# Kernel tuning notes

Measured on AMD Instinct MI355X. Metric: run time of the kernel, lower is better.

Reference implementation:

```python
import jax, jax.numpy as jnp
from jax import lax
import numpy as np

B = 32768
N_IN = 8
N_HID = 64
N_CTRL = 2
M_SCEN = (1.0, 1.2)          # scenario parameters for f/g
M_NOM = 1.0
CLF_LAM = 1.0
CBF_LAM = 1.0
P_CLF = 100.0
P_CBF = 50.0
QP_ITERS = 80                # fixed-iteration batched ADMM (OSQP-style) replacing CvxpyLayer
RHO = 1.0
SIGMA = 1e-6
INF = jnp.inf


def setup_inputs() -> dict:
    key = jax.random.key(0)
    ks = jax.random.split(key, 16)
    s = 0.3
    return {
        "x":   jax.random.normal(ks[0], (B, N_IN), jnp.float32),
        "VW1": jax.random.normal(ks[1], (N_HID, N_IN), jnp.float32) * s,
        "Vb1": jax.random.normal(ks[2], (N_HID,), jnp.float32) * s,
        "VW2": jax.random.normal(ks[3], (N_HID, N_HID), jnp.float32) * s,
        "Vb2": jax.random.normal(ks[4], (N_HID,), jnp.float32) * s,
        "HW1": jax.random.normal(ks[5], (N_HID, N_IN), jnp.float32) * s,
        "Hb1": jax.random.normal(ks[6], (N_HID,), jnp.float32) * s,
        "HW2": jax.random.normal(ks[7], (N_HID, N_HID), jnp.float32) * s,
        "Hb2": jax.random.normal(ks[8], (N_HID,), jnp.float32) * s,
        "HW3": jax.random.normal(ks[9], (N_HID, N_HID), jnp.float32) * s,
        "Hb3": jax.random.normal(ks[10], (N_HID,), jnp.float32) * s,
        "HW4": jax.random.normal(ks[11], (1, N_HID), jnp.float32) * s,
        "Hb4": jax.random.normal(ks[12], (1,), jnp.float32) * s,
        "G0":  jax.random.normal(ks[13], (N_IN, N_CTRL), jnp.float32) * s,
        "K":   jax.random.normal(ks[14], (N_IN, N_CTRL), jnp.float32) * s,
    }


def _lyapunov(x, W1, b1, W2, b2):
    t1 = jnp.tanh(x @ W1.T + b1)                                   # [B,H]
    t2 = jnp.tanh(t1 @ W2.T + b2)                                  # [B,H]
    V = 0.5 * jnp.sum(t2 * t2, axis=1)                             # [B]
    # fused diag(1-t^2) @ W chain (no diag_embed materialization)
    D1 = (1.0 - t1 ** 2)[:, :, None] * W1[None]                    # [B,H,N]
    D2 = (1.0 - t2 ** 2)[:, :, None] * jnp.einsum('hk,bkn->bhn', W2, D1)
    grad_V = jnp.einsum('bh,bhn->bn', t2, D2)                      # [B,N]
    return V, grad_V


def _barrier(x, W1, b1, W2, b2, W3, b3, W4, b4):
    t1 = jnp.tanh(x @ W1.T + b1)
    t2 = jnp.tanh(t1 @ W2.T + b2)
    t3 = jnp.tanh(t2 @ W3.T + b3)
    H = t3 @ W4.T + b4                                             # [B,1]
    D1 = (1.0 - t1 ** 2)[:, :, None] * W1[None]
    D2 = (1.0 - t2 ** 2)[:, :, None] * jnp.einsum('hk,bkn->bhn', W2, D1)
    D3 = (1.0 - t3 ** 2)[:, :, None] * jnp.einsum('hk,bkn->bhn', W3, D2)
    grad_H = jnp.einsum('oh,bhn->bn', W4, D3)                      # [B,N] (o=1)
    return H, grad_H


def _solve_qp(q, A, lo, hi):
    """Batched OSQP-style ADMM for min 0.5 z^T P z + q^T z  s.t. lo <= A z <= hi.
    P = diag([2,2,0,0,0,0]); z = [u(2), r_clf(2), s_cbf(2)]. Fixed iterations."""
    nb, mc, nz = A.shape[0], A.shape[1], A.shape[2]
    Pdiag = jnp.array([2.0, 2.0, 0.0, 0.0, 0.0, 0.0], q.dtype)
    M = RHO * jnp.einsum('bmi,bmj->bij', A, A) + jnp.diag(Pdiag + SIGMA)
    Minv = jnp.linalg.inv(M)                                       # [B,6,6]
    x0 = jnp.zeros((nb, nz), q.dtype)
    z0 = jnp.zeros((nb, mc), q.dtype)
    y0 = jnp.zeros((nb, mc), q.dtype)

    def step(carry, _):
        xx, zz, yy = carry
        rhs = SIGMA * xx - q + jnp.einsum('bmi,bm->bi', A, RHO * zz - yy)
        xt = jnp.einsum('bij,bj->bi', Minv, rhs)
        zt = jnp.einsum('bmi,bi->bm', A, xt)
        zn = jnp.clip(zt + yy / RHO, lo, hi)
        yn = yy + RHO * (zt - zn)
        return (xt, zn, yn), None

    (xf, _, _), _ = lax.scan(step, (x0, z0, y0), None, length=QP_ITERS)
    return xf                                                      # [B,6]


def _forward(x, VW1, Vb1, VW2, Vb2, HW1, Hb1, HW2, Hb2, HW3, Hb3, HW4, Hb4, G0, K):
    V, grad_V = _lyapunov(x, VW1, Vb1, VW2, Vb2)
    H, grad_H = _barrier(x, HW1, Hb1, HW2, Hb2, HW3, Hb3, HW4, Hb4)

    LfVs, LgVs, LfHs, LgHs = [], [], [], []
    for m in M_SCEN:
        # f(x,m) = -x/m ; g(x,m) = G0/m
        LfVs.append(-jnp.sum(grad_V * x, axis=1) / m)              # [B]
        LgVs.append((grad_V @ G0) / m)                             # [B,C]
        LfHs.append(-jnp.sum(grad_H * x, axis=1) / m)
        LgHs.append((grad_H @ G0) / m)
    u_nom = -(x @ K) * (1.0 / M_NOM)                               # [B,C]

    nb = x.shape[0]
    z2 = jnp.zeros((nb, 2), x.dtype)
    ey = jnp.eye(2, dtype=x.dtype)
    e = lambda i: jnp.broadcast_to(ey[i], (nb, 2))
    ninf = jnp.full((nb,), -INF, x.dtype)
    pinf = jnp.full((nb,), INF, x.dtype)
    zer = jnp.zeros((nb,), x.dtype)

    rows, los, his = [], [], []
    for i in range(len(M_SCEN)):
        # CBF: LfH + LgH@u + cbf_lam*H + s_i >= 0
        rows.append(jnp.concatenate([LgHs[i], z2, e(i)], axis=1))
        los.append(-(LfHs[i] + CBF_LAM * H[:, 0])); his.append(pinf)
        # CLF: LfV + LgV@u + clf_lam*V - r_i <= 0
        rows.append(jnp.concatenate([LgVs[i], -e(i), z2], axis=1))
        los.append(ninf); his.append(-(LfVs[i] + CLF_LAM * V))
    for i in range(len(M_SCEN)):
        rows.append(jnp.concatenate([z2, e(i), z2], axis=1)); los.append(zer); his.append(pinf)
    for i in range(len(M_SCEN)):
        rows.append(jnp.concatenate([z2, z2, e(i)], axis=1)); los.append(zer); his.append(pinf)

    A = jnp.stack(rows, axis=1)                                    # [B,8,6]
    lo = jnp.stack(los, axis=1)                                    # [B,8]
    hi = jnp.stack(his, axis=1)
    # objective ||u-u_nom||^2 + p_clf*sum r + p_cbf*sum s  ->  q = [-2 u_nom, p_clf, p_clf, p_cbf, p_cbf]
    q = jnp.concatenate([-2.0 * u_nom,
                         jnp.full((nb, 2), P_CLF, x.dtype),
                         jnp.full((nb, 2), P_CBF, x.dtype)], axis=1)

    z = _solve_qp(q, A, lo, hi)                                    # [B,6]
    u = z[:, :N_CTRL]
    relaxation = jnp.mean(z[:, N_CTRL:N_CTRL + len(M_SCEN)], axis=1, keepdims=True)  # [B,1]

    ns = float(len(M_SCEN))
    Vdot = sum(LfVs[i] + jnp.sum(LgVs[i] * u, axis=1) for i in range(len(M_SCEN))) / ns
    Hdot = sum(LfHs[i] + jnp.sum(LgHs[i] * u, axis=1) for i in range(len(M_SCEN))) / ns
    return u, relaxation, V, Vdot[:, None, None], H, Hdot[:, None, None]


def reference(x, VW1, Vb1, VW2, Vb2, HW1, Hb1, HW2, Hb2, HW3, Hb3, HW4, Hb4, G0, K):
    return _forward(x, VW1, Vb1, VW2, Vb2, HW1, Hb1, HW2, Hb2, HW3, Hb3, HW4, Hb4, G0, K)
```

## Files before the change

### kernel.cpp

```cpp
#include <hip/hip_runtime.h>
#include <hip/hip_bf16.h>
#include <math.h>

#define BTOT 32768

typedef _Float16 f16x8 __attribute__((ext_vector_type(8)));
typedef _Float16 f16x4 __attribute__((ext_vector_type(4)));
typedef float    f32x4 __attribute__((ext_vector_type(4)));

#define LDS_FENCE() asm volatile("s_waitcnt lgkmcnt(0)" ::: "memory")

__device__ __forceinline__ float ldin(const void* p, int i, int f32f) {
  return f32f ? ((const float*)p)[i]
              : __bfloat162float(((const __hip_bfloat16*)p)[i]);
}

__device__ __forceinline__ f32x4 MFMA(f16x8 a, f16x8 b, f32x4 c) {
  return __builtin_amdgcn_mfma_f32_16x16x32_f16(a, b, c, 0, 0, 0);
}

__device__ __forceinline__ float tanh_fast(float x) {
  float e = __expf(2.f * x);
  return 1.f - 2.f * __builtin_amdgcn_rcpf(e + 1.f);
}

__device__ __forceinline__ float redq(float v) {
  v += __shfl_xor(v, 16, 64);
  v += __shfl_xor(v, 32, 64);
  return v;
}

__device__ __forceinline__ int widx(int h, int k) {
  return ((h >> 4) << 10) + ((k >> 5) << 9) + (((k >> 3) & 3) << 7) + ((h & 15) << 3) + (k & 7);
}

__global__ __launch_bounds__(512, 4) void fused_kernel(
    const void* px, const void* pVW1, const void* pVb1, const void* pVW2, const void* pVb2,
    const void* pHW1, const void* pHb1, const void* pHW2, const void* pHb2,
    const void* pHW3, const void* pHb3, const void* pHW4, const void* pHb4,
    const void* pG0, const void* pK, float* out)
{
  __shared__ __align__(16) _Float16 sVW2[4096], sVW2T[4096];
  __shared__ __align__(16) _Float16 sHW2[4096], sHW2T[4096];
  __shared__ __align__(16) _Float16 sHW3[4096], sHW3T[4096];
  __shared__ __align__(16) _Float16 sW1Vh[512], sW1Vl[512], sW1Hh[512], sW1Hl[512];
  __shared__ __align__(16) _Float16 sAct[8][1024];
  __shared__ __align__(16) float sVb1[64], sVb2[64], sHb1[64], sHb2[64], sHb3[64], sW4[64];
  __shared__ __align__(16) float sWGV0[64], sWGV1[64], sWGH0[64], sWGH1[64];
  __shared__ __align__(16) float sQP[128][11];
  __shared__ float sKv[16], sHb4v;
  __shared__ int sCnt;

  const int tid = threadIdx.x, lane = tid & 63, wave = tid >> 6;
  const int m = lane & 15, q = lane >> 4;
  const int ro = q * 128 + m * 8;

  if (tid == 0) sCnt = 0;
  __syncthreads();
  {
    const unsigned short* xb = (const unsigned short*)px;
    int good = 0;
#pragma unroll
    for (int i = 0; i < 2; ++i) {
      int ex = (xb[tid * 2 + i] >> 7) & 0xFF;
      good += (ex >= 97 && ex <= 157) ? 1 : 0;
    }
    atomicAdd(&sCnt, good);
  }
  __syncthreads();
  const int f32f = (sCnt >= 870) ? 0 : 1;
  const bool wsplit = (f32f != 0);

  for (int i = tid; i < 4096; i += 512) {
    int h = i >> 6, k = i & 63;
    int fw = widx(h, k), tw = widx(k, h);
    sVW2[fw] = (_Float16)ldin(pVW2, i, f32f); sVW2T[tw] = sVW2[fw];
    sHW2[fw] = (_Float16)ldin(pHW2, i, f32f); sHW2T[tw] = sHW2[fw];
    sHW3[fw] = (_Float16)ldin(pHW3, i, f32f); sHW3T[tw] = sHW3[fw];
  }
  for (int i = tid; i < 512; i += 512) {
    float v = ldin(pVW1, i, f32f); _Float16 hh = (_Float16)v;
    sW1Vh[i] = hh; sW1Vl[i] = (_Float16)(v - (float)hh);
    v = ldin(pHW1, i, f32f); hh = (_Float16)v;
    sW1Hh[i] = hh; sW1Hl[i] = (_Float16)(v - (float)hh);
  }
  if (tid < 64) {
    float a0 = 0.f, a1 = 0.f, b0 = 0.f, b1 = 0.f;
#pragma unroll
    for (int nn = 0; nn < 8; ++nn) {
      float g0 = ldin(pG0, 2 * nn, f32f), g1 = ldin(pG0, 2 * nn + 1, f32f);
      float wv = ldin(pVW1, tid * 8 + nn, f32f), wh = ldin(pHW1, tid * 8 + nn, f32f);
      a0 += wv * g0; a1 += wv * g1; b0 += wh * g0; b1 += wh * g1;
    }
    sWGV0[tid] = a0; sWGV1[tid] = a1; sWGH0[tid] = b0; sWGH1[tid] = b1;
    sVb1[tid] = ldin(pVb1, tid, f32f);
    sVb2[tid] = ldin(pVb2, tid, f32f);
    sHb1[tid] = ldin(pHb1, tid, f32f);
    sHb2[tid] = ldin(pHb2, tid, f32f);
    sHb3[tid] = ldin(pHb3, tid, f32f);
    sW4[tid]  = ldin(pHW4, tid, f32f);
  }
  if (tid < 16) sKv[tid] = ldin(pK, tid, f32f);
  if (tid == 0) sHb4v = ldin(pHb4, 0, f32f);
  __syncthreads();

  f16x8 zf;
#pragma unroll
  for (int i = 0; i < 8; ++i) zf[i] = (_Float16)0.f;

  _Float16* act = sAct[wave];
  const int tb = wave * 16;
  const int e0 = blockIdx.x * 128 + tb;

  f16x8 xbh = zf, xbl = zf;
  if (lane < 16) {
#pragma unroll
    for (int n = 0; n < 8; ++n) {
      float v = ldin(px, (e0 + m) * 8 + n, f32f);
      _Float16 hh = (_Float16)v;
      xbh[n] = hh; xbl[n] = (_Float16)(v - (float)hh);
    }
  }

  auto wgemm = [&](const _Float16* Wp, f32x4* acc) {
    f16x8 b0 = *(const f16x8*)(act + ro);
    f16x8 b1 = *(const f16x8*)(act + 512 + ro);
#pragma unroll
    for (int ht = 0; ht < 4; ++ht) {
      const _Float16* ap = Wp + ht * 1024 + ro;
      f32x4 c = {0.f, 0.f, 0.f, 0.f};
      c = MFMA(*(const f16x8*)ap, b0, c);
      c = MFMA(*(const f16x8*)(ap + 512), b1, c);
      acc[ht] = c;
    }
  };
  auto wstore = [&](const f32x4* vals) {
#pragma unroll
    for (int ht = 0; ht < 4; ++ht) {
      int aw = ((ht >> 1) << 9) + (((ht & 1) * 2 + (q >> 1)) << 7) + m * 8 + ((q & 1) << 2);
      f16x4 vh;
#pragma unroll
      for (int r = 0; r < 4; ++r) vh[r] = (_Float16)vals[ht][r];
      *(f16x4*)(act + aw) = vh;
    }
  };
  auto l1gemm = [&](const _Float16* W1h, const _Float16* W1l, f32x4* acc) {
#pragma unroll
    for (int ht = 0; ht < 4; ++ht) {
      f16x8 afh = zf, afl = zf;
      if (lane < 16) {
        afh = *(const f16x8*)(W1h + (ht * 16 + m) * 8);
        afl = *(const f16x8*)(W1l + (ht * 16 + m) * 8);
      }
      f32x4 c = {0.f, 0.f, 0.f, 0.f};
      c = MFMA(afh, xbh, c);
      c = MFMA(afh, xbl, c);
      if (wsplit) c = MFMA(afl, xbh, c);
      acc[ht] = c;
    }
  };

  f32x4 acc[4], z1[4], d1[4], d2[4], tv[4];

  l1gemm(sW1Vh, sW1Vl, acc);
#pragma unroll
  for (int ht = 0; ht < 4; ++ht) {
    z1[ht] = acc[ht];
    f32x4 b4 = *(const f32x4*)&sVb1[ht * 16 + q * 4];
#pragma unroll
    for (int r = 0; r < 4; ++r) {
      float t = tanh_fast(z1[ht][r] + b4[r]);
      tv[ht][r] = t; d1[ht][r] = 1.f - t * t;
    }
  }
  wstore(tv); LDS_FENCE();

  wgemm(sVW2, acc);
  float pV = 0.f;
#pragma unroll
  for (int ht = 0; ht < 4; ++ht) {
    f32x4 b4 = *(const f32x4*)&sVb2[ht * 16 + q * 4];
#pragma unroll
    for (int r = 0; r < 4; ++r) {
      float t = tanh_fast(acc[ht][r] + b4[r]);
      pV += t * t;
      tv[ht][r] = t * (1.f - t * t);
    }
  }
  wstore(tv); LDS_FENCE();

  wgemm(sVW2T, acc);
  float pgvx = 0.f, plv0 = 0.f, plv1 = 0.f;
#pragma unroll
  for (int ht = 0; ht < 4; ++ht) {
    f32x4 g0 = *(const f32x4*)&sWGV0[ht * 16 + q * 4];
    f32x4 g1 = *(const f32x4*)&sWGV1[ht * 16 + q * 4];
#pragma unroll
    for (int r = 0; r < 4; ++r) {
      float wt = acc[ht][r] * d1[ht][r];
      pgvx += wt * z1[ht][r];
      plv0 += wt * g0[r]; plv1 += wt * g1[r];
    }
  }

  l1gemm(sW1Hh, sW1Hl, acc);
#pragma unroll
  for (int ht = 0; ht < 4; ++ht) {
    z1[ht] = acc[ht];
    f32x4 b4 = *(const f32x4*)&sHb1[ht * 16 + q * 4];
#pragma unroll
    for (int r = 0; r < 4; ++r) {
      float t = tanh_fast(z1[ht][r] + b4[r]);
      tv[ht][r] = t; d1[ht][r] = 1.f - t * t;
    }
  }
  wstore(tv); LDS_FENCE();

  wgemm(sHW2, acc);
#pragma unroll
  for (int ht = 0; ht < 4; ++ht) {
    f32x4 b4 = *(const f32x4*)&sHb2[ht * 16 + q * 4];
#pragma unroll
    for (int r = 0; r < 4; ++r) {
      float t = tanh_fast(acc[ht][r] + b4[r]);
      tv[ht][r] = t; d2[ht][r] = 1.f - t * t;
    }
  }
  wstore(tv); LDS_FENCE();

  wgemm(sHW3, acc);
  float pH = 0.f;
#pragma unroll
  for (int ht = 0; ht < 4; ++ht) {
    f32x4 b4 = *(const f32x4*)&sHb3[ht * 16 + q * 4];
    f32x4 w4 = *(const f32x4*)&sW4[ht * 16 + q * 4];
#pragma unroll
    for (int r = 0; r < 4; ++r) {
      float t = tanh_fast(acc[ht][r] + b4[r]);
      pH += t * w4[r];
      tv[ht][r] = w4[r] * (1.f - t * t);
    }
  }
  wstore(tv); LDS_FENCE();

  wgemm(sHW3T, acc);
#pragma unroll
  for (int ht = 0; ht < 4; ++ht)
#pragma unroll
    for (int r = 0; r < 4; ++r) tv[ht][r] = acc[ht][r] * d2[ht][r];
  wstore(tv); LDS_FENCE();

  wgemm(sHW2T, acc);
  float pghx = 0.f, plh0 = 0.f, plh1 = 0.f;
#pragma unroll
  for (int ht = 0; ht < 4; ++ht) {
    f32x4 g0 = *(const f32x4*)&sWGH0[ht * 16 + q * 4];
    f32x4 g1 = *(const f32x4*)&sWGH1[ht * 16 + q * 4];
#pragma unroll
    for (int r = 0; r < 4; ++r) {
      float wt = acc[ht][r] * d1[ht][r];
      pghx += wt * z1[ht][r];
      plh0 += wt * g0[r]; plh1 += wt * g1[r];
    }
  }

  {
    float rgvx = redq(pgvx), rlv0 = redq(plv0), rlv1 = redq(plv1), rV = 0.5f * redq(pV);
    float rghx = redq(pghx), rlh0 = redq(plh0), rlh1 = redq(plh1), rH = redq(pH) + sHb4v;
    if (lane < 16) {
      int el = tb + lane;
      sQP[el][0] = rlh0;  sQP[el][1] = rlh1;
      sQP[el][2] = rlv0;  sQP[el][3] = rlv1;
      sQP[el][4] = rghx;  sQP[el][5] = rgvx;
      sQP[el][6] = rV;    sQP[el][7] = rH;
      out[98304 + e0 + lane]  = rV;
      out[163840 + e0 + lane] = rH;
    }
  }
  __syncthreads();

  if (tid >= 128) return;
  const int e = blockIdx.x * 128 + tid;
  const float im = 1.0f / 1.2f;
  const float sg = 1e-6f;

  float gh0 = sQP[tid][0], gh1 = sQP[tid][1];
  float gv0 = sQP[tid][2], gv1 = sQP[tid][3];
  float ghx = sQP[tid][4], gvx = sQP[tid][5];
  float V   = sQP[tid][6], H   = sQP[tid][7];

  float un0 = 0.f, un1 = 0.f;
#pragma unroll
  for (int n = 0; n < 8; ++n) {
    float xv = ldin(px, e * 8 + n, f32f);
    un0 -= xv * sKv[2 * n];
    un1 -= xv * sKv[2 * n + 1];
  }

  float lo0 = ghx - H;
  float hi1 = gvx - V;
  float lo2 = ghx * im - H;
  float hi3 = gvx * im - V;
  float qv0 = -2.f * un0, qv1 = -2.f * un1;

  const float d  = 2.f + sg;
  const float rd = 1.f / d;
  const float al = 1.f + im * im;
  const float be = al * (1.f - rd);
  float S00 = be * (gh0 * gh0 + gv0 * gv0) + d;
  float S11 = be * (gh1 * gh1 + gv1 * gv1) + d;
  float S01 = be * (gh0 * gh1 + gv0 * gv1);
  float idet = 1.f / (S00 * S11 - S01 * S01);
  float i00 = S11 * idet, i11 = S00 * idet, i01 = -S01 * idet;

  float X0 = 0.f, X1 = 0.f, X2 = 0.f, X3 = 0.f, X4 = 0.f, X5 = 0.f;
  float Z[8] = {0.f, 0.f, 0.f, 0.f, 0.f, 0.f, 0.f, 0.f};
  float Y[8] = {0.f, 0.f, 0.f, 0.f, 0.f, 0.f, 0.f, 0.f};

#pragma unroll 1
  for (int it = 0; it < 80; ++it) {
    float t0 = Z[0] - Y[0], t1 = Z[1] - Y[1], t2 = Z[2] - Y[2], t3 = Z[3] - Y[3];
    float t4 = Z[4] - Y[4], t5 = Z[5] - Y[5], t6 = Z[6] - Y[6], t7 = Z[7] - Y[7];
    float tauh = t0 + im * t2, tauv = t1 + im * t3;
    float b0 = sg * X0 - qv0 + gh0 * tauh + gv0 * tauv;
    float b1 = sg * X1 - qv1 + gh1 * tauh + gv1 * tauv;
    float b2 = sg * X2 - 100.f - t1 + t4;
    float b3 = sg * X3 - 100.f - t3 + t5;
    float b4 = sg * X4 - 50.f + t0 + t6;
    float b5 = sg * X5 - 50.f + t2 + t7;
    float p  = b2 + im * b3;
    float s2 = b4 + im * b5;
    float cb0 = gh0 * s2 - gv0 * p;
    float cb1 = gh1 * s2 - gv1 * p;
    float u0b = b0 - cb0 * rd;
    float u1b = b1 - cb1 * rd;
    X0 = i00 * u0b + i01 * u1b;
    X1 = i01 * u0b + i11 * u1b;
    float gdH = gh0 * X0 + gh1 * X1;
    float gdV = gv0 * X0 + gv1 * X1;
    X2 = (b2 + gdV) * rd;
    X3 = (b3 + im * gdV) * rd;
    X4 = (b4 - gdH) * rd;
    X5 = (b5 - im * gdH) * rd;
    float zt0 = gdH + X4;
    float zt1 = gdV - X2;
    float zt2 = gdH * im + X5;
    float zt3 = gdV * im - X3;

    float v, zn;
    v = zt0 + Y[0]; zn = fmaxf(v, lo0); Y[0] += zt0 - zn; Z[0] = zn;
    v = zt1 + Y[1]; zn = fminf(v, hi1); Y[1] += zt1 - zn; Z[1] = zn;
    v = zt2 + Y[2]; zn = fmaxf(v, lo2); Y[2] += zt2 - zn; Z[2] = zn;
    v = zt3 + Y[3]; zn = fminf(v, hi3); Y[3] += zt3 - zn; Z[3] = zn;
    v = X2 + Y[4];  zn = fmaxf(v, 0.f); Y[4] += X2 - zn;  Z[4] = zn;
    v = X3 + Y[5];  zn = fmaxf(v, 0.f); Y[5] += X3 - zn;  Z[5] = zn;
    v = X4 + Y[6];  zn = fmaxf(v, 0.f); Y[6] += X4 - zn;  Z[6] = zn;
    v = X5 + Y[7];  zn = fmaxf(v, 0.f); Y[7] += X5 - zn;  Z[7] = zn;
  }

  float relax = 0.5f * (X2 + X3);
  const float cc = 0.5f * (1.f + im);
  float Vdot = cc * (gv0 * X0 + gv1 * X1 - gvx);
  float Hdot = cc * (gh0 * X0 + gh1 * X1 - ghx);

  out[2 * e]      = X0;
  out[2 * e + 1]  = X1;
  out[65536 + e]  = relax;
  out[131072 + e] = Vdot;
  out[196608 + e] = Hdot;
}

extern "C" void kernel_launch(void* const* d_in, const int* in_sizes, int n_in,
                              void* d_out, int out_size, void* d_ws, size_t ws_size,
                              hipStream_t stream) {
  float* out = (float*)d_out;
  fused_kernel<<<256, 512, 0, stream>>>(
      d_in[0], d_in[1], d_in[2], d_in[3], d_in[4],
      d_in[5], d_in[6], d_in[7], d_in[8],
      d_in[9], d_in[10], d_in[11], d_in[12],
      d_in[13], d_in[14], out);
}
```

Measured before the change: 121.6 us.

## Split weight prep into separate kernel and process 16 rows per small block

Weight conversion and transposition to f16 MFMA layout moves into a prep kernel that writes to workspace, so each block no longer redoes it in shared memory. The main kernel now uses 2048 blocks of 128 threads, each handling 16 rows with the hidden dimension split across two waves. The V and H networks are interleaved so their independent GEMMs can overlap, and weights are read from global memory/cache instead of LDS. The cost is an extra launch, block-level barriers between layers, and a final QP stage that uses only 16 threads per block.

```diff
diff --git a/kernel.cpp b/kernel.cpp
--- a/kernel.cpp
+++ b/kernel.cpp
@@ -7,8 +7,6 @@
 typedef _Float16 f16x8 __attribute__((ext_vector_type(8)));
 typedef _Float16 f16x4 __attribute__((ext_vector_type(4)));
 typedef float    f32x4 __attribute__((ext_vector_type(4)));
-
-#define LDS_FENCE() asm volatile("s_waitcnt lgkmcnt(0)" ::: "memory")
 
 __device__ __forceinline__ float ldin(const void* p, int i, int f32f) {
   return f32f ? ((const float*)p)[i]
@@ -34,27 +32,23 @@
   return ((h >> 4) << 10) + ((k >> 5) << 9) + (((k >> 3) & 3) << 7) + ((h & 15) << 3) + (k & 7);
 }
 
-__global__ __launch_bounds__(512, 4) void fused_kernel(
-    const void* px, const void* pVW1, const void* pVb1, const void* pVW2, const void* pVb2,
-    const void* pHW1, const void* pHb1, const void* pHW2, const void* pHb2,
-    const void* pHW3, const void* pHb3, const void* pHW4, const void* pHb4,
-    const void* pG0, const void* pK, float* out)
+#define OFF_VW2   0
+#define OFF_VW2T  4096
+#define OFF_HW2   8192
+#define OFF_HW2T  12288
+#define OFF_HW3   16384
+#define OFF_HW3T  20480
+#define OFF_W1VH  24576
+#define OFF_W1VL  25088
+#define OFF_W1HH  25600
+#define OFF_W1HL  26112
+
+__global__ __launch_bounds__(256) void prep_kernel(
+    const void* px, const void* pVW1, const void* pVW2,
+    const void* pHW1, const void* pHW2, const void* pHW3, _Float16* wsp)
 {
-  __shared__ __align__(16) _Float16 sVW2[4096], sVW2T[4096];
-  __shared__ __align__(16) _Float16 sHW2[4096], sHW2T[4096];
-  __shared__ __align__(16) _Float16 sHW3[4096], sHW3T[4096];
-  __shared__ __align__(16) _Float16 sW1Vh[512], sW1Vl[512], sW1Hh[512], sW1Hl[512];
-  __shared__ __align__(16) _Float16 sAct[8][1024];
-  __shared__ __align__(16) float sVb1[64], sVb2[64], sHb1[64], sHb2[64], sHb3[64], sW4[64];
-  __shared__ __align__(16) float sWGV0[64], sWGV1[64], sWGH0[64], sWGH1[64];
-  __shared__ __align__(16) float sQP[128][11];
-  __shared__ float sKv[16], sHb4v;
   __shared__ int sCnt;
-
-  const int tid = threadIdx.x, lane = tid & 63, wave = tid >> 6;
-  const int m = lane & 15, q = lane >> 4;
-  const int ro = q * 128 + m * 8;
-
+  const int tid = threadIdx.x;
   if (tid == 0) sCnt = 0;
   __syncthreads();
   {
@@ -68,22 +62,58 @@
     atomicAdd(&sCnt, good);
   }
   __syncthreads();
-  const int f32f = (sCnt >= 870) ? 0 : 1;
+  const int f32f = (sCnt >= 435) ? 0 : 1;
+
+  const int t = blockIdx.x * 256 + tid;
+  int h = t >> 6, k = t & 63;
+  int fw = widx(h, k), tw = widx(k, h);
+  _Float16 v;
+  v = (_Float16)ldin(pVW2, t, f32f); wsp[OFF_VW2 + fw] = v; wsp[OFF_VW2T + tw] = v;
+  v = (_Float16)ldin(pHW2, t, f32f); wsp[OFF_HW2 + fw] = v; wsp[OFF_HW2T + tw] = v;
+  v = (_Float16)ldin(pHW3, t, f32f); wsp[OFF_HW3 + fw] = v; wsp[OFF_HW3T + tw] = v;
+  if (t < 512) {
+    float f = ldin(pVW1, t, f32f); _Float16 hh = (_Float16)f;
+    wsp[OFF_W1VH + t] = hh; wsp[OFF_W1VL + t] = (_Float16)(f - (float)hh);
+    f = ldin(pHW1, t, f32f); hh = (_Float16)f;
+    wsp[OFF_W1HH + t] = hh; wsp[OFF_W1HL + t] = (_Float16)(f - (float)hh);
+  }
+}
+
+__global__ __launch_bounds__(128, 4) void main_kernel(
+    const void* px, const void* pVb1, const void* pVb2,
+    const void* pHb1, const void* pHb2, const void* pHb3,
+    const void* pHW4, const void* pHb4, const void* pG0, const void* pK,
+    const void* pVW1, const void* pHW1,
+    const _Float16* wsp, float* out)
+{
+  __shared__ __align__(16) _Float16 actV[1024], actH[1024];
+  __shared__ __align__(16) float sQPp[2][16][8];
+  __shared__ __align__(16) float sVb1[64], sVb2[64], sHb1[64], sHb2[64], sHb3[64], sW4[64];
+  __shared__ __align__(16) float sWGV0[64], sWGV1[64], sWGH0[64], sWGH1[64];
+  __shared__ float sKv[16], sHb4v;
+  __shared__ int sCnt;
+
+  const int tid = threadIdx.x, lane = tid & 63, wave = tid >> 6;
+  const int m = lane & 15, q = lane >> 4;
+  const int ro = lane * 8;
+  const int e0 = blockIdx.x * 16;
+
+  if (tid == 0) sCnt = 0;
+  __syncthreads();
+  {
+    const unsigned short* xb = (const unsigned short*)px;
+    int good = 0;
+#pragma unroll
+    for (int i = 0; i < 4; ++i) {
+      int ex = (xb[tid * 4 + i] >> 7) & 0xFF;
+      good += (ex >= 97 && ex <= 157) ? 1 : 0;
+    }
+    atomicAdd(&sCnt, good);
+  }
+  __syncthreads();
+  const int f32f = (sCnt >= 435) ? 0 : 1;
   const bool wsplit = (f32f != 0);
 
-  for (int i = tid; i < 4096; i += 512) {
-    int h = i >> 6, k = i & 63;
-    int fw = widx(h, k), tw = widx(k, h);
-    sVW2[fw] = (_Float16)ldin(pVW2, i, f32f); sVW2T[tw] = sVW2[fw];
-    sHW2[fw] = (_Float16)ldin(pHW2, i, f32f); sHW2T[tw] = sHW2[fw];
-    sHW3[fw] = (_Float16)ldin(pHW3, i, f32f); sHW3T[tw] = sHW3[fw];
-  }
-  for (int i = tid; i < 512; i += 512) {
-    float v = ldin(pVW1, i, f32f); _Float16 hh = (_Float16)v;
-    sW1Vh[i] = hh; sW1Vl[i] = (_Float16)(v - (float)hh);
-    v = ldin(pHW1, i, f32f); hh = (_Float16)v;
-    sW1Hh[i] = hh; sW1Hl[i] = (_Float16)(v - (float)hh);
-  }
   if (tid < 64) {
     float a0 = 0.f, a1 = 0.f, b0 = 0.f, b1 = 0.f;
 #pragma unroll
@@ -102,15 +132,10 @@
   }
   if (tid < 16) sKv[tid] = ldin(pK, tid, f32f);
   if (tid == 0) sHb4v = ldin(pHb4, 0, f32f);
-  __syncthreads();
 
   f16x8 zf;
 #pragma unroll
   for (int i = 0; i < 8; ++i) zf[i] = (_Float16)0.f;
-
-  _Float16* act = sAct[wave];
-  const int tb = wave * 16;
-  const int e0 = blockIdx.x * 128 + tb;
 
   f16x8 xbh = zf, xbl = zf;
   if (lane < 16) {
@@ -121,173 +146,165 @@
       xbh[n] = hh; xbl[n] = (_Float16)(v - (float)hh);
     }
   }
-
-  auto wgemm = [&](const _Float16* Wp, f32x4* acc) {
-    f16x8 b0 = *(const f16x8*)(act + ro);
-    f16x8 b1 = *(const f16x8*)(act + 512 + ro);
-#pragma unroll
-    for (int ht = 0; ht < 4; ++ht) {
-      const _Float16* ap = Wp + ht * 1024 + ro;
+  __syncthreads();
+
+  auto hgemm = [&](int poff, const _Float16* a_, f32x4* acc) {
+    f16x8 b0 = *(const f16x8*)(a_ + ro);
+    f16x8 b1 = *(const f16x8*)(a_ + 512 + ro);
+#pragma unroll
+    for (int i = 0; i < 2; ++i) {
+      const _Float16* ap = wsp + poff + (2 * wave + i) * 1024 + ro;
       f32x4 c = {0.f, 0.f, 0.f, 0.f};
       c = MFMA(*(const f16x8*)ap, b0, c);
       c = MFMA(*(const f16x8*)(ap + 512), b1, c);
-      acc[ht] = c;
+      acc[i] = c;
     }
   };
-  auto wstore = [&](const f32x4* vals) {
-#pragma unroll
-    for (int ht = 0; ht < 4; ++ht) {
+  auto wstore = [&](const f32x4* vals, _Float16* a_) {
+#pragma unroll
+    for (int i = 0; i < 2; ++i) {
+      int ht = 2 * wave + i;
       int aw = ((ht >> 1) << 9) + (((ht & 1) * 2 + (q >> 1)) << 7) + m * 8 + ((q & 1) << 2);
       f16x4 vh;
 #pragma unroll
-      for (int r = 0; r < 4; ++r) vh[r] = (_Float16)vals[ht][r];
-      *(f16x4*)(act + aw) = vh;
+      for (int r = 0; r < 4; ++r) vh[r] = (_Float16)vals[i][r];
+      *(f16x4*)(a_ + aw) = vh;
     }
   };
-  auto l1gemm = [&](const _Float16* W1h, const _Float16* W1l, f32x4* acc) {
-#pragma unroll
-    for (int ht = 0; ht < 4; ++ht) {
+  auto l1gemm = [&](int hoff, int loff, f32x4* acc) {
+#pragma unroll
+    for (int i = 0; i < 2; ++i) {
+      int ht = 2 * wave + i;
       f16x8 afh = zf, afl = zf;
       if (lane < 16) {
-        afh = *(const f16x8*)(W1h + (ht * 16 + m) * 8);
-        afl = *(const f16x8*)(W1l + (ht * 16 + m) * 8);
+        afh = *(const f16x8*)(wsp + hoff + (ht * 16 + m) * 8);
+        afl = *(const f16x8*)(wsp + loff + (ht * 16 + m) * 8);
       }
       f32x4 c = {0.f, 0.f, 0.f, 0.f};
       c = MFMA(afh, xbh, c);
       c = MFMA(afh, xbl, c);
       if (wsplit) c = MFMA(afl, xbh, c);
-      acc[ht] = c;
+      acc[i] = c;
     }
   };
 
-  f32x4 acc[4], z1[4], d1[4], d2[4], tv[4];
-
-  l1gemm(sW1Vh, sW1Vl, acc);
-#pragma unroll
-  for (int ht = 0; ht < 4; ++ht) {
-    z1[ht] = acc[ht];
-    f32x4 b4 = *(const f32x4*)&sVb1[ht * 16 + q * 4];
+  f32x4 accV[2], accH[2], z1V[2], z1H[2], d1V[2], d1H[2], d2H[2], tvV[2], tvH[2];
+
+  l1gemm(OFF_W1VH, OFF_W1VL, accV);
+  l1gemm(OFF_W1HH, OFF_W1HL, accH);
+#pragma unroll
+  for (int i = 0; i < 2; ++i) {
+    int hb = (2 * wave + i) * 16 + q * 4;
+    z1V[i] = accV[i]; z1H[i] = accH[i];
+    f32x4 bV = *(const f32x4*)&sVb1[hb];
+    f32x4 bH = *(const f32x4*)&sHb1[hb];
 #pragma unroll
     for (int r = 0; r < 4; ++r) {
-      float t = tanh_fast(z1[ht][r] + b4[r]);
-      tv[ht][r] = t; d1[ht][r] = 1.f - t * t;
-    }
-  }
-  wstore(tv); LDS_FENCE();
-
-  wgemm(sVW2, acc);
+      float t = tanh_fast(z1V[i][r] + bV[r]);
+      tvV[i][r] = t; d1V[i][r] = 1.f - t * t;
+      t = tanh_fast(z1H[i][r] + bH[r]);
+      tvH[i][r] = t; d1H[i][r] = 1.f - t * t;
+    }
+  }
+  wstore(tvV, actV); wstore(tvH, actH);
+  __syncthreads();
+
+  hgemm(OFF_VW2, actV, accV);
+  hgemm(OFF_HW2, actH, accH);
   float pV = 0.f;
 #pragma unroll
-  for (int ht = 0; ht < 4; ++ht) {
-    f32x4 b4 = *(const f32x4*)&sVb2[ht * 16 + q * 4];
+  for (int i = 0; i < 2; ++i) {
+    int hb = (2 * wave + i) * 16 + q * 4;
+    f32x4 bV = *(const f32x4*)&sVb2[hb];
+    f32x4 bH = *(const f32x4*)&sHb2[hb];
 #pragma unroll
     for (int r = 0; r < 4; ++r) {
-      float t = tanh_fast(acc[ht][r] + b4[r]);
+      float t = tanh_fast(accV[i][r] + bV[r]);
       pV += t * t;
-      tv[ht][r] = t * (1.f - t * t);
-    }
-  }
-  wstore(tv); LDS_FENCE();
-
-  wgemm(sVW2T, acc);
-  float pgvx = 0.f, plv0 = 0.f, plv1 = 0.f;
-#pragma unroll
-  for (int ht = 0; ht < 4; ++ht) {
-    f32x4 g0 = *(const f32x4*)&sWGV0[ht * 16 + q * 4];
-    f32x4 g1 = *(const f32x4*)&sWGV1[ht * 16 + q * 4];
+      tvV[i][r] = t * (1.f - t * t);
+      t = tanh_fast(accH[i][r] + bH[r]);
+      tvH[i][r] = t; d2H[i][r] = 1.f - t * t;
+    }
+  }
+  __syncthreads();
+  wstore(tvV, actV); wstore(tvH, actH);
+  __syncthreads();
+
+  hgemm(OFF_VW2T, actV, accV);
+  hgemm(OFF_HW3, actH, accH);
+  float pgvx = 0.f, plv0 = 0.f, plv1 = 0.f, pH = 0.f;
+#pragma unroll
+  for (int i = 0; i < 2; ++i) {
+    int hb = (2 * wave + i) * 16 + q * 4;
+    f32x4 g0 = *(const f32x4*)&sWGV0[hb];
+    f32x4 g1 = *(const f32x4*)&sWGV1[hb];
+    f32x4 bH = *(const f32x4*)&sHb3[hb];
+    f32x4 w4 = *(const f32x4*)&sW4[hb];
 #pragma unroll
     for (int r = 0; r < 4; ++r) {
-      float wt = acc[ht][r] * d1[ht][r];
-      pgvx += wt * z1[ht][r];
+      float wt = accV[i][r] * d1V[i][r];
+      pgvx += wt * z1V[i][r];
       plv0 += wt * g0[r]; plv1 += wt * g1[r];
-    }
-  }
-
-  l1gemm(sW1Hh, sW1Hl, acc);
-#pragma unroll
-  for (int ht = 0; ht < 4; ++ht) {
-    z1[ht] = acc[ht];
-    f32x4 b4 = *(const f32x4*)&sHb1[ht * 16 + q * 4];
+      float t = tanh_fast(accH[i][r] + bH[r]);
+      pH += t * w4[r];
+      tvH[i][r] = w4[r] * (1.f - t * t);
+    }
+  }
+  __syncthreads();
+  wstore(tvH, actH);
+  __syncthreads();
+
+  hgemm(OFF_HW3T, actH, accH);
+#pragma unroll
+  for (int i = 0; i < 2; ++i)
+#pragma unroll
+    for (int r = 0; r < 4; ++r) tvH[i][r] = accH[i][r] * d2H[i][r];
+  __syncthreads();
+  wstore(tvH, actH);
+  __syncthreads();
+
+  hgemm(OFF_HW2T, actH, accH);
+  float pghx = 0.f, plh0 = 0.f, plh1 = 0.f;
+#pragma unroll
+  for (int i = 0; i < 2; ++i) {
+    int hb = (2 * wave + i) * 16 + q * 4;
+    f32x4 g0 = *(const f32x4*)&sWGH0[hb];
+    f32x4 g1 = *(const f32x4*)&sWGH1[hb];
 #pragma unroll
     for (int r = 0; r < 4; ++r) {
-      float t = tanh_fast(z1[ht][r] + b4[r]);
-      tv[ht][r] = t; d1[ht][r] = 1.f - t * t;
-    }
-  }
-  wstore(tv); LDS_FENCE();
-
-  wgemm(sHW2, acc);
-#pragma unroll
-  for (int ht = 0; ht < 4; ++ht) {
-    f32x4 b4 = *(const f32x4*)&sHb2[ht * 16 + q * 4];
-#pragma unroll
-    for (int r = 0; r < 4; ++r) {
-      float t = tanh_fast(acc[ht][r] + b4[r]);
-      tv[ht][r] = t; d2[ht][r] = 1.f - t * t;
-    }
-  }
-  wstore(tv); LDS_FENCE();
-
-  wgemm(sHW3, acc);
-  float pH = 0.f;
-#pragma unroll
-  for (int ht = 0; ht < 4; ++ht) {
-    f32x4 b4 = *(const f32x4*)&sHb3[ht * 16 + q * 4];
-    f32x4 w4 = *(const f32x4*)&sW4[ht * 16 + q * 4];
-#pragma unroll
-    for (int r = 0; r < 4; ++r) {
-      float t = tanh_fast(acc[ht][r] + b4[r]);
-      pH += t * w4[r];
-      tv[ht][r] = w4[r] * (1.f - t * t);
-    }
-  }
-  wstore(tv); LDS_FENCE();
-
-  wgemm(sHW3T, acc);
-#pragma unroll
-  for (int ht = 0; ht < 4; ++ht)
-#pragma unroll
-    for (int r = 0; r < 4; ++r) tv[ht][r] = acc[ht][r] * d2[ht][r];
-  wstore(tv); LDS_FENCE();
-
-  wgemm(sHW2T, acc);
-  float pghx = 0.f, plh0 = 0.f, plh1 = 0.f;
-#pragma unroll
-  for (int ht = 0; ht < 4; ++ht) {
-    f32x4 g0 = *(const f32x4*)&sWGH0[ht * 16 + q * 4];
-    f32x4 g1 = *(const f32x4*)&sWGH1[ht * 16 + q * 4];
-#pragma unroll
-    for (int r = 0; r < 4; ++r) {
-      float wt = acc[ht][r] * d1[ht][r];
-      pghx += wt * z1[ht][r];
+      float wt = accH[i][r] * d1H[i][r];
+      pghx += wt * z1H[i][r];
       plh0 += wt * g0[r]; plh1 += wt * g1[r];
     }
   }
 
   {
-    float rgvx = redq(pgvx), rlv0 = redq(plv0), rlv1 = redq(plv1), rV = 0.5f * redq(pV);
-    float rghx = redq(pghx), rlh0 = redq(plh0), rlh1 = redq(plh1), rH = redq(pH) + sHb4v;
+    float a0 = redq(plh0), a1 = redq(plh1), a2 = redq(plv0), a3 = redq(plv1);
+    float a4 = redq(pghx), a5 = redq(pgvx), a6 = redq(pV), a7 = redq(pH);
     if (lane < 16) {
-      int el = tb + lane;
-      sQP[el][0] = rlh0;  sQP[el][1] = rlh1;
-      sQP[el][2] = rlv0;  sQP[el][3] = rlv1;
-      sQP[el][4] = rghx;  sQP[el][5] = rgvx;
-      sQP[el][6] = rV;    sQP[el][7] = rH;
-      out[98304 + e0 + lane]  = rV;
-      out[163840 + e0 + lane] = rH;
-    }
-  }
-  __syncthreads();
-
-  if (tid >= 128) return;
-  const int e = blockIdx.x * 128 + tid;
+      sQPp[wave][lane][0] = a0; sQPp[wave][lane][1] = a1;
+      sQPp[wave][lane][2] = a2; sQPp[wave][lane][3] = a3;
+      sQPp[wave][lane][4] = a4; sQPp[wave][lane][5] = a5;
+      sQPp[wave][lane][6] = a6; sQPp[wave][lane][7] = a7;
+    }
+  }
+  __syncthreads();
+
+  if (tid >= 16) return;
+  const int e = e0 + tid;
+  float gh0 = sQPp[0][tid][0] + sQPp[1][tid][0];
+  float gh1 = sQPp[0][tid][1] + sQPp[1][tid][1];
+  float gv0 = sQPp[0][tid][2] + sQPp[1][tid][2];
+  float gv1 = sQPp[0][tid][3] + sQPp[1][tid][3];
+  float ghx = sQPp[0][tid][4] + sQPp[1][tid][4];
+  float gvx = sQPp[0][tid][5] + sQPp[1][tid][5];
+  float V   = 0.5f * (sQPp[0][tid][6] + sQPp[1][tid][6]);
+  float H   = sQPp[0][tid][7] + sQPp[1][tid][7] + sHb4v;
+  out[98304 + e]  = V;
+  out[163840 + e] = H;
+
   const float im = 1.0f / 1.2f;
   const float sg = 1e-6f;
-
-  float gh0 = sQP[tid][0], gh1 = sQP[tid][1];
-  float gv0 = sQP[tid][2], gv1 = sQP[tid][3];
-  float ghx = sQP[tid][4], gvx = sQP[tid][5];
-  float V   = sQP[tid][6], H   = sQP[tid][7];
 
   float un0 = 0.f, un1 = 0.f;
 #pragma unroll
@@ -374,9 +391,12 @@
                               void* d_out, int out_size, void* d_ws, size_t ws_size,
                               hipStream_t stream) {
   float* out = (float*)d_out;
-  fused_kernel<<<256, 512, 0, stream>>>(
-      d_in[0], d_in[1], d_in[2], d_in[3], d_in[4],
-      d_in[5], d_in[6], d_in[7], d_in[8],
-      d_in[9], d_in[10], d_in[11], d_in[12],
-      d_in[13], d_in[14], out);
-}
+  _Float16* wsp = (_Float16*)d_ws;
+  prep_kernel<<<16, 256, 0, stream>>>(
+      d_in[0], d_in[1], d_in[3], d_in[5], d_in[7], d_in[9], wsp);
+  main_kernel<<<2048, 128, 0, stream>>>(
+      d_in[0], d_in[2], d_in[4], d_in[6], d_in[8], d_in[10],
+      d_in[11], d_in[12], d_in[13], d_in[14],
+      d_in[1], d_in[5],
+      wsp, out);
+}
```

Measured after the change: 127.9 us. 5.1% more time.
